# Kernel tuning notes

Hardware: AMD Instinct MI355X
Metric: run time of the kernel (lower is better)

Reference implementation:

```python
import jax, jax.numpy as jnp
import numpy as np

B, N, D = 2, 4096, 2048
H, DH, W = 8, 128, 512          # heads (num_queries), dim_head, window_size
SCALE = 8.0                      # qk_scale (qk_rmsnorm=True)


def setup_inputs() -> dict:
    key = jax.random.key(0)
    ks = jax.random.split(key, 5)
    return {
        "x": jax.random.normal(ks[0], (B, N, D), jnp.float32),
        "Wq": jax.random.normal(ks[1], (H * DH, D), jnp.float32) * 0.02,
        "Wkv": jax.random.normal(ks[2], (2 * H * DH, D), jnp.float32) * 0.02,
        "q_scale": jnp.ones((DH,), jnp.float32),
        "k_scale": jnp.ones((DH,), jnp.float32),
        "Wg": jax.random.normal(ks[3], (H, D), jnp.float32) * 0.02,
        "bg": jnp.zeros((H,), jnp.float32),
        "Wo": jax.random.normal(ks[4], (D, H * DH), jnp.float32) * 0.02,
    }


def _l2norm(t):
    # F.normalize: x / max(||x||, eps)
    return t / jnp.maximum(jnp.linalg.norm(t, axis=-1, keepdims=True), 1e-12)


def reference(x, Wq, Wkv, q_scale, k_scale, Wg, bg, Wo):
    b, n, _ = x.shape
    inner = H * DH
    q = (x @ Wq.T).reshape(b, n, H, DH).transpose(0, 2, 1, 3)      # b h n d
    kv = x @ Wkv.T
    k = kv[..., :inner].reshape(b, n, H, DH).transpose(0, 2, 1, 3)
    v = kv[..., inner:].reshape(b, n, H, DH).transpose(0, 2, 1, 3)
    # qk rmsnorm
    q = _l2norm(q) * q_scale
    k = _l2norm(k) * k_scale

    nb = n // W
    qb = q.reshape(b, H, nb, W, DH)
    kb = k.reshape(b, H, nb, W, DH)
    vb = v.reshape(b, H, nb, W, DH)

    def look_around(t):  # prepend previous bucket (look_backward=1)
        prev = jnp.concatenate([jnp.zeros_like(t[:, :, :1]), t[:, :, :-1]], axis=2)
        return jnp.concatenate([prev, t], axis=3)  # b h nb 2W d

    kw, vw = look_around(kb), look_around(vb)

    pos = jnp.arange(n).reshape(nb, W)
    pos_prev = jnp.concatenate([jnp.full((1, W), -1), pos[:-1]], axis=0)
    posk = jnp.concatenate([pos_prev, pos], axis=1)                 # nb 2W
    dist = pos[:, :, None] - posk[:, None, :]                       # nb W 2W
    # causal + exact window: attend j with 0 <= i - j <= W, valid (non-pad) key
    mask = (posk[:, None, :] >= 0) & (dist >= 0) & (dist <= W)

    sim = jnp.einsum('bhnid,bhnjd->bhnij', qb * SCALE, kw)
    sim = jnp.where(mask, sim, jnp.finfo(sim.dtype).min)
    attn = jax.nn.softmax(sim, axis=-1)
    o = jnp.einsum('bhnij,bhnjd->bhnid', attn, vw).reshape(b, H, n, DH)

    # per-head sigmoid value gating
    gates = jax.nn.sigmoid(jnp.einsum('bnd,hd->bhn', x, Wg) + bg[None, :, None])
    o = o * gates[..., None]

    o = o.transpose(0, 2, 1, 3).reshape(b, n, inner)                # b n (h d)
    return o @ Wo.T
```

## Files before the change

### kernel.cpp

```cpp
#include <hip/hip_runtime.h>
#include <hip/hip_bf16.h>
#include <cstdint>

typedef short short8 __attribute__((ext_vector_type(8)));
typedef __bf16 bf16x8 __attribute__((ext_vector_type(8)));
typedef float f32x4 __attribute__((ext_vector_type(4)));
typedef unsigned short u16;
typedef unsigned int u32;

#define B_  2
#define N_  4096
#define D_  2048
#define H_  8
#define DH_ 128
#define W_  512
#define M_  (B_*N_)
#define INNER_ (H_*DH_)

static __device__ __forceinline__ u16 f2bf(float f) {
  u32 u = __float_as_uint(f);
  u32 r = (u + 0x7fffu + ((u >> 16) & 1u)) >> 16;
  return (u16)r;
}
static __device__ __forceinline__ float bf2f(u16 u) {
  return __uint_as_float(((u32)u) << 16);
}
static __device__ __forceinline__ f32x4 mfma16(short8 a, short8 b, f32x4 c) {
  return __builtin_amdgcn_mfma_f32_16x16x32_bf16(
      __builtin_bit_cast(bf16x8, a), __builtin_bit_cast(bf16x8, b), c, 0, 0, 0);
}

#define GLOAD_LDS16(g, s) \
  __builtin_amdgcn_global_load_lds((const __attribute__((address_space(1))) void*)(g), \
                                   (__attribute__((address_space(3))) void*)(s), 16, 0, 0)

__global__ __launch_bounds__(256) void cvt_kernel(
    const float* __restrict__ x, const float* __restrict__ Wq,
    const float* __restrict__ Wkv, const float* __restrict__ Wo,
    u16* __restrict__ xb, u16* __restrict__ Wcat, u16* __restrict__ Wob) {
  size_t i = ((size_t)blockIdx.x * 256 + threadIdx.x) * 8;
  const float* src; u16* dst; size_t off;
  const size_t SX = 16777216ul, SQ = 2097152ul, SKV = 4194304ul;
  if (i < SX)                { src = x;   dst = xb;             off = i; }
  else if (i < SX+SQ)        { src = Wq;  dst = Wcat;           off = i - SX; }
  else if (i < SX+SQ+SKV)    { src = Wkv; dst = Wcat + 2097152; off = i - SX - SQ; }
  else                       { src = Wo;  dst = Wob;            off = i - SX - SQ - SKV; }
  float4 a = *(const float4*)(src + off);
  float4 b = *(const float4*)(src + off + 4);
  short8 o;
  o[0]=(short)f2bf(a.x); o[1]=(short)f2bf(a.y); o[2]=(short)f2bf(a.z); o[3]=(short)f2bf(a.w);
  o[4]=(short)f2bf(b.x); o[5]=(short)f2bf(b.y); o[6]=(short)f2bf(b.z); o[7]=(short)f2bf(b.w);
  *(short8*)(dst + off) = o;
}

template<int EPI>
__global__ __launch_bounds__(256) void gemm_bt(
    const u16* __restrict__ A, const u16* __restrict__ Bw,
    u16* __restrict__ Dq, u16* __restrict__ Dk, u16* __restrict__ Dv,
    float* __restrict__ Cf, int N, int K) {
  __shared__ u16 sA[128*64];
  __shared__ u16 sB[128*64];
  const int tid = threadIdx.x;
  const int lane = tid & 63, wv = tid >> 6;
  const int wm = wv >> 1, wn = wv & 1;
  const int m0 = blockIdx.y * 128, n0 = blockIdx.x * 128;
  const int l15 = lane & 15, l4 = lane >> 4;
  f32x4 acc[4][4] = {};

  #pragma unroll 1
  for (int kt = 0; kt < K; kt += 64) {
    __syncthreads();
    #pragma unroll
    for (int r = 0; r < 4; ++r) {
      int cf = r*256 + tid;
      int row = cf >> 3, cph = cf & 7;
      int clg = cph ^ (row & 7);
      GLOAD_LDS16(A + (size_t)(m0 + row)*K + kt + clg*8, sA + (size_t)(r*256 + wv*64)*8);
    }
    #pragma unroll
    for (int r = 0; r < 4; ++r) {
      int cf = r*256 + tid;
      int row = cf >> 3, cph = cf & 7;
      int clg = cph ^ (row & 7);
      GLOAD_LDS16(Bw + (size_t)(n0 + row)*K + kt + clg*8, sB + (size_t)(r*256 + wv*64)*8);
    }
    __syncthreads();
    #pragma unroll
    for (int ks = 0; ks < 2; ++ks) {
      short8 af[4], bfr[4];
      #pragma unroll
      for (int mf = 0; mf < 4; ++mf) {
        int row = wm*64 + mf*16 + l15;
        int ch = (ks*4 + l4) ^ (row & 7);
        af[mf] = *(const short8*)(sA + row*64 + ch*8);
      }
      #pragma unroll
      for (int nf = 0; nf < 4; ++nf) {
        int row = wn*64 + nf*16 + l15;
        int ch = (ks*4 + l4) ^ (row & 7);
        bfr[nf] = *(const short8*)(sB + row*64 + ch*8);
      }
      #pragma unroll
      for (int mf = 0; mf < 4; ++mf)
        #pragma unroll
        for (int nf = 0; nf < 4; ++nf)
          acc[mf][nf] = mfma16(af[mf], bfr[nf], acc[mf][nf]);
    }
  }

  if (EPI == 0) {
    const int bufsel = blockIdx.x >> 3;
    const int h = blockIdx.x & 7;
    u16* dst = bufsel == 0 ? Dq : (bufsel == 1 ? Dk : Dv);
    #pragma unroll
    for (int mf = 0; mf < 4; ++mf)
      #pragma unroll
      for (int nf = 0; nf < 4; ++nf)
        #pragma unroll
        for (int j = 0; j < 4; ++j) {
          int m = m0 + wm*64 + mf*16 + l4*4 + j;
          int d = wn*64 + nf*16 + l15;
          int b = m >> 12, n = m & (N_ - 1);
          dst[(((size_t)(b*H_ + h)*N_ + n) << 7) + d] = f2bf(acc[mf][nf][j]);
        }
  } else {
    #pragma unroll
    for (int mf = 0; mf < 4; ++mf)
      #pragma unroll
      for (int nf = 0; nf < 4; ++nf)
        #pragma unroll
        for (int j = 0; j < 4; ++j) {
          int m = m0 + wm*64 + mf*16 + l4*4 + j;
          int nn = n0 + wn*64 + nf*16 + l15;
          Cf[(size_t)m*N + nn] = acc[mf][nf][j];
        }
  }
}

__global__ __launch_bounds__(256) void normqk_kernel(
    u16* __restrict__ qb, u16* __restrict__ kb,
    const float* __restrict__ qs, const float* __restrict__ ks) {
  int lane = threadIdx.x & 63, wv = threadIdx.x >> 6;
  size_t vec = (size_t)blockIdx.x * 4 + wv;
  bool isq = vec < 65536;
  u16* p = isq ? qb + vec*128 : kb + (vec - 65536)*128;
  const float* sc = isq ? qs : ks;
  u32 u = *(const u32*)(p + lane*2);
  float a = bf2f((u16)(u & 0xffffu));
  float b = bf2f((u16)(u >> 16));
  float ss = a*a + b*b;
  #pragma unroll
  for (int off = 32; off >= 1; off >>= 1) ss += __shfl_xor(ss, off);
  float inv = 1.0f / fmaxf(sqrtf(ss), 1e-12f);
  if (isq) inv *= 8.0f;
  float r0 = a * inv * sc[lane*2];
  float r1 = b * inv * sc[lane*2 + 1];
  *(u32*)(p + lane*2) = (u32)f2bf(r0) | ((u32)f2bf(r1) << 16);
}

__global__ __launch_bounds__(256) void transpose_v_kernel(
    const u16* __restrict__ v, u16* __restrict__ vT) {
  int bh = blockIdx.x >> 6;
  int n0 = (blockIdx.x & 63) << 6;
  __shared__ u16 tl[64][136];
  int tid = threadIdx.x;
  #pragma unroll
  for (int r = 0; r < 4; ++r) {
    int cf = r*256 + tid;
    int row = cf >> 4, ch = cf & 15;
    *(short8*)&tl[row][ch*8] = *(const short8*)(v + ((size_t)bh*N_ + n0 + row)*128 + ch*8);
  }
  __syncthreads();
  #pragma unroll
  for (int r = 0; r < 4; ++r) {
    int cf = r*256 + tid;
    int d = cf >> 3, nch = cf & 7;
    short8 o;
    #pragma unroll
    for (int i = 0; i < 8; ++i) o[i] = (short)tl[nch*8 + i][d];
    *(short8*)(vT + ((size_t)bh*128 + d)*N_ + n0 + nch*8) = o;
  }
}

__global__ __launch_bounds__(256) void gates_kernel(
    const float* __restrict__ x, const float* __restrict__ Wg,
    const float* __restrict__ bg, float* __restrict__ gates) {
  int m = blockIdx.x;
  int tid = threadIdx.x;
  const float* xr = x + (size_t)m * D_;
  float acc[8] = {};
  for (int d = tid; d < D_; d += 256) {
    float xv = xr[d];
    #pragma unroll
    for (int h = 0; h < 8; ++h) acc[h] = fmaf(xv, Wg[h*D_ + d], acc[h]);
  }
  #pragma unroll
  for (int h = 0; h < 8; ++h)
    #pragma unroll
    for (int off = 32; off >= 1; off >>= 1) acc[h] += __shfl_xor(acc[h], off);
  __shared__ float red[4][8];
  int lane = tid & 63, wv = tid >> 6;
  if (lane == 0) {
    #pragma unroll
    for (int h = 0; h < 8; ++h) red[wv][h] = acc[h];
  }
  __syncthreads();
  if (tid < 8) {
    float vsum = red[0][tid] + red[1][tid] + red[2][tid] + red[3][tid] + bg[tid];
    gates[(size_t)m*8 + tid] = 1.0f / (1.0f + __expf(-vsum));
  }
}

__global__ __launch_bounds__(256) void attn_kernel(
    const u16* __restrict__ q, const u16* __restrict__ k,
    const u16* __restrict__ vT, const float* __restrict__ gates,
    u16* __restrict__ o) {
  const int bid = blockIdx.x;
  const int t = bid & 3;
  const int c = (bid >> 2) & 7;
  const int bh = bid >> 5;
  const int b = bh >> 3, h = bh & 7;
  const int i0 = c*W_ + t*128;
  const int tid = threadIdx.x;
  const int lane = tid & 63, wv = tid >> 6;
  const int l15 = lane & 15, l4 = lane >> 4;

  __shared__ u16 sK[64*128];
  __shared__ u16 sV[128*64];
  __shared__ u16 sP[4][32*64];

  short8 qf[2][4];
  const u16* qbase = q + (((size_t)bh*N_ + i0 + wv*32) << 7);
  #pragma unroll
  for (int mf = 0; mf < 2; ++mf)
    #pragma unroll
    for (int ks = 0; ks < 4; ++ks)
      qf[mf][ks] = *(const short8*)(qbase + (mf*16 + l15)*128 + ks*32 + l4*8);

  float mrow[2][4], lrow[2][4];
  f32x4 oacc[2][8];
  #pragma unroll
  for (int mf = 0; mf < 2; ++mf) {
    #pragma unroll
    for (int j = 0; j < 4; ++j) { mrow[mf][j] = -1e30f; lrow[mf][j] = 0.f; }
    #pragma unroll
    for (int df = 0; df < 8; ++df) oacc[mf][df] = (f32x4){0.f,0.f,0.f,0.f};
  }
  u16* sPw = &sP[wv][0];

  #pragma unroll 1
  for (int kt = 0; kt < 10; ++kt) {
    const int j0 = i0 - 512 + kt*64;
    if (j0 < 0) continue;
    __syncthreads();
    #pragma unroll
    for (int r = 0; r < 4; ++r) {
      int cf = r*256 + tid;
      int row = cf >> 4, cph = cf & 15;
      int clg = cph ^ (row & 15);
      GLOAD_LDS16(k + (((size_t)bh*N_ + j0 + row) << 7) + clg*8, sK + (size_t)(r*256 + wv*64)*8);
    }
    #pragma unroll
    for (int r = 0; r < 4; ++r) {
      int cf = r*256 + tid;
      int row = cf >> 3, cph = cf & 7;
      int clg = cph ^ (row & 7);
      GLOAD_LDS16(vT + ((size_t)bh*128 + row)*N_ + j0 + clg*8, sV + (size_t)(r*256 + wv*64)*8);
    }
    __syncthreads();

    f32x4 s[2][4];
    #pragma unroll
    for (int mf = 0; mf < 2; ++mf)
      #pragma unroll
      for (int nf = 0; nf < 4; ++nf) s[mf][nf] = (f32x4){0.f,0.f,0.f,0.f};
    #pragma unroll
    for (int ks = 0; ks < 4; ++ks) {
      short8 kb[4];
      #pragma unroll
      for (int nf = 0; nf < 4; ++nf) {
        int row = nf*16 + l15;
        int ch = (ks*4 + l4) ^ (row & 15);
        kb[nf] = *(const short8*)(sK + row*128 + ch*8);
      }
      #pragma unroll
      for (int mf = 0; mf < 2; ++mf)
        #pragma unroll
        for (int nf = 0; nf < 4; ++nf)
          s[mf][nf] = mfma16(qf[mf][ks], kb[nf], s[mf][nf]);
    }

    if (kt < 2 || kt > 7) {
      #pragma unroll
      for (int mf = 0; mf < 2; ++mf)
        #pragma unroll
        for (int nf = 0; nf < 4; ++nf)
          #pragma unroll
          for (int j = 0; j < 4; ++j) {
            int r = wv*32 + mf*16 + l4*4 + j;
            int sidx = nf*16 + l15;
            int dist = (i0 + r) - (j0 + sidx);
            if (dist < 0 || dist > 512) s[mf][nf][j] = -1e30f;
          }
    }

    #pragma unroll
    for (int mf = 0; mf < 2; ++mf) {
      #pragma unroll
      for (int j = 0; j < 4; ++j) {
        float mx = fmaxf(fmaxf(s[mf][0][j], s[mf][1][j]), fmaxf(s[mf][2][j], s[mf][3][j]));
        #pragma unroll
        for (int off = 1; off <= 8; off <<= 1) mx = fmaxf(mx, __shfl_xor(mx, off));
        float mnew = fmaxf(mrow[mf][j], mx);
        float scal = __expf(mrow[mf][j] - mnew);
        mrow[mf][j] = mnew;
        float ls = 0.f;
        #pragma unroll
        for (int nf = 0; nf < 4; ++nf) {
          float p = __expf(s[mf][nf][j] - mnew);
          s[mf][nf][j] = p;
          ls += p;
        }
        #pragma unroll
        for (int off = 1; off <= 8; off <<= 1) ls += __shfl_xor(ls, off);
        lrow[mf][j] = lrow[mf][j]*scal + ls;
        #pragma unroll
        for (int df = 0; df < 8; ++df) oacc[mf][df][j] *= scal;
        int prow = mf*16 + l4*4 + j;
        #pragma unroll
        for (int nf = 0; nf < 4; ++nf) {
          int pcol = nf*16 + l15;
          int ch = (pcol >> 3) ^ (prow & 7);
          sPw[prow*64 + ch*8 + (pcol & 7)] = f2bf(s[mf][nf][j]);
        }
      }
    }

    #pragma unroll
    for (int ks2 = 0; ks2 < 2; ++ks2) {
      short8 pa[2];
      #pragma unroll
      for (int mf = 0; mf < 2; ++mf) {
        int prow = mf*16 + l15;
        int ch = (ks2*4 + l4) ^ (prow & 7);
        pa[mf] = *(const short8*)(sPw + prow*64 + ch*8);
      }
      #pragma unroll
      for (int df = 0; df < 8; ++df) {
        int vd = df*16 + l15;
        int ch2 = (ks2*4 + l4) ^ (vd & 7);
        short8 vb = *(const short8*)(sV + vd*64 + ch2*8);
        #pragma unroll
        for (int mf = 0; mf < 2; ++mf)
          oacc[mf][df] = mfma16(pa[mf], vb, oacc[mf][df]);
      }
    }
  }

  #pragma unroll
  for (int mf = 0; mf < 2; ++mf)
    #pragma unroll
    for (int j = 0; j < 4; ++j) {
      int r = wv*32 + mf*16 + l4*4 + j;
      int i = i0 + r;
      float f = (1.0f / lrow[mf][j]) * gates[((size_t)b*N_ + i)*8 + h];
      #pragma unroll
      for (int df = 0; df < 8; ++df)
        o[((size_t)b*N_ + i)*INNER_ + h*128 + df*16 + l15] = f2bf(oacc[mf][df][j] * f);
    }
}

extern "C" void kernel_launch(void* const* d_in, const int* in_sizes, int n_in,
                              void* d_out, int out_size, void* d_ws, size_t ws_size,
                              hipStream_t stream) {
  const float* x       = (const float*)d_in[0];
  const float* Wq      = (const float*)d_in[1];
  const float* Wkv     = (const float*)d_in[2];
  const float* q_scale = (const float*)d_in[3];
  const float* k_scale = (const float*)d_in[4];
  const float* Wg      = (const float*)d_in[5];
  const float* bg      = (const float*)d_in[6];
  const float* Wo      = (const float*)d_in[7];
  float* out = (float*)d_out;

  u16* qb  = (u16*)d_out;
  u16* kb  = qb + 8388608;
  u16* vb  = kb + 8388608;
  u16* vTb = vb + 8388608;

  char* w = (char*)d_ws;
  u16* xb   = (u16*)w;
  u16* ob   = (u16*)w;
  u16* Wcat = (u16*)(w + 33554432);
  u16* Wob  = (u16*)(w + 46137344);
  float* gb = (float*)(w + 50331648);
  (void)in_sizes; (void)n_in; (void)out_size; (void)ws_size;

  cvt_kernel<<<12288, 256, 0, stream>>>(x, Wq, Wkv, Wo, xb, Wcat, Wob);
  gemm_bt<0><<<dim3(24, 64), 256, 0, stream>>>(xb, Wcat, qb, kb, vb, nullptr, 3072, 2048);
  normqk_kernel<<<32768, 256, 0, stream>>>(qb, kb, q_scale, k_scale);
  transpose_v_kernel<<<1024, 256, 0, stream>>>(vb, vTb);
  gates_kernel<<<8192, 256, 0, stream>>>(x, Wg, bg, gb);
  attn_kernel<<<512, 256, 0, stream>>>(qb, kb, vTb, gb, ob);
  gemm_bt<1><<<dim3(16, 64), 256, 0, stream>>>(ob, Wob, nullptr, nullptr, nullptr, out, 2048, 1024);
}
```

Measured before the change: 314.7 us.

## Replace GEMM with 256x256-tile, 8-wave, multi-stage pipelined LDS kernel

Replaces the 128x128 single-buffered GEMM with a 256x256 tile, 512-thread kernel. It uses 128 KB of dynamic LDS split into three stages of 32-wide K half-tiles, issues global-to-LDS prefetches interleaved with the MFMA phases, and raises MFMA priority with s_setprio. Blocks are remapped with an XCD-aware swizzle for L2 locality, and the QKV epilogue now derives head and buffer per column. The goal is to hide load latency and raise arithmetic intensity in both projection GEMMs. In exchange the kernel has heavier register and LDS pressure and relies on hand-placed waitcnt and barrier choreography with hardcoded grid assumptions (by = swz & 31).

Result: faster. 308.3 us (-2.1%).

```diff
diff --git a/kernel.cpp b/kernel.cpp
--- a/kernel.cpp
+++ b/kernel.cpp
@@ -53,86 +53,121 @@
   *(short8*)(dst + off) = o;
 }
 
+#define BARRIER() __builtin_amdgcn_s_barrier()
+#define WAIT_LGKM0() do { asm volatile("s_waitcnt lgkmcnt(0)" ::: "memory"); \
+                          __builtin_amdgcn_sched_barrier(0); } while(0)
+#define WAIT_VM4() asm volatile("s_waitcnt vmcnt(4)" ::: "memory")
+#define WAIT_VM0() asm volatile("s_waitcnt vmcnt(0)" ::: "memory")
+
+#define STAGE_HALF(gbase, sreg) do { \
+    const u16* _g = (gbase) + _cs; \
+    GLOAD_LDS16(_g + (size_t)(wv*32 + (lane>>2))*K,      (sreg) + wv*1024); \
+    GLOAD_LDS16(_g + (size_t)(wv*32 + 16 + (lane>>2))*K, (sreg) + wv*1024 + 512); \
+  } while(0)
+
+#define LOAD_AF(sreg, mfb) do { \
+    _Pragma("unroll") for (int q = 0; q < 4; ++q) \
+      af[q] = *(const short8*)((sreg) + (wm*128 + ((mfb)+q)*16 + l15)*32 + fch); \
+  } while(0)
+#define LOAD_BF(sreg) do { \
+    _Pragma("unroll") for (int q = 0; q < 4; ++q) \
+      bf[q] = *(const short8*)((sreg) + (wn*64 + q*16 + l15)*32 + fch); \
+  } while(0)
+
+#define PH_MFMA(mfb) do { \
+    __builtin_amdgcn_s_setprio(1); \
+    _Pragma("unroll") for (int q = 0; q < 4; ++q) \
+      _Pragma("unroll") for (int nf = 0; nf < 4; ++nf) \
+        acc[(mfb)+q][nf] = mfma16(af[q], bf[nf], acc[(mfb)+q][nf]); \
+    __builtin_amdgcn_s_setprio(0); \
+  } while(0)
+
+#define TILE4(T, SA_C, SB_C, SA_N, SB_N, C1, C2) do { \
+    const u16* gAt = gA + (size_t)(T)*64; \
+    const u16* gBt = gB + (size_t)(T)*64; \
+    short8 af[4], bf[4]; \
+    LOAD_AF(SA_C, 0); LOAD_BF(SB_C); \
+    if (C1) STAGE_HALF(gAt + 96, (SA_N) + 8192); \
+    BARRIER(); WAIT_LGKM0(); PH_MFMA(0); BARRIER(); \
+    LOAD_AF(SA_C, 4); \
+    if (C1) STAGE_HALF(gBt + 96, (SB_N) + 8192); \
+    BARRIER(); WAIT_LGKM0(); PH_MFMA(4); BARRIER(); \
+    LOAD_AF((SA_C) + 8192, 0); LOAD_BF((SB_C) + 8192); \
+    if (C2) STAGE_HALF(gAt + 128, SA_C); \
+    BARRIER(); WAIT_LGKM0(); PH_MFMA(0); BARRIER(); \
+    LOAD_AF((SA_C) + 8192, 4); \
+    if (C2) { STAGE_HALF(gBt + 128, SB_C); WAIT_VM4(); } else { WAIT_VM0(); } \
+    BARRIER(); WAIT_LGKM0(); PH_MFMA(4); BARRIER(); \
+  } while(0)
+
 template<int EPI>
-__global__ __launch_bounds__(256) void gemm_bt(
+__global__ __launch_bounds__(512, 2) void gemm256(
     const u16* __restrict__ A, const u16* __restrict__ Bw,
     u16* __restrict__ Dq, u16* __restrict__ Dk, u16* __restrict__ Dv,
-    float* __restrict__ Cf, int N, int K) {
-  __shared__ u16 sA[128*64];
-  __shared__ u16 sB[128*64];
+    float* __restrict__ Cf, int Ncols, int K) {
+  extern __shared__ u16 lds[];
   const int tid = threadIdx.x;
   const int lane = tid & 63, wv = tid >> 6;
-  const int wm = wv >> 1, wn = wv & 1;
-  const int m0 = blockIdx.y * 128, n0 = blockIdx.x * 128;
+  const int wm = wv >> 2, wn = wv & 3;
   const int l15 = lane & 15, l4 = lane >> 4;
-  f32x4 acc[4][4] = {};
-
+
+  const int nwg = gridDim.x;
+  const int swz = (blockIdx.x & 7) * (nwg >> 3) + (blockIdx.x >> 3);
+  const int by = swz & 31;
+  const int bx = swz >> 5;
+  const int m0 = by << 8, n0 = bx << 8;
+
+  const u16* gA = A + (size_t)m0 * K;
+  const u16* gB = Bw + (size_t)n0 * K;
+  u16* sA0 = lds;
+  u16* sB0 = lds + 32768;
+
+  const int _cs = ((lane & 3) ^ ((lane >> 3) & 3)) * 8;
+  const int fch = (l4 ^ ((l15 >> 1) & 3)) * 8;
+
+  f32x4 acc[8][4] = {};
+
+  STAGE_HALF(gA,      sA0);
+  STAGE_HALF(gB,      sB0);
+  STAGE_HALF(gA + 32, sA0 + 8192);
+  STAGE_HALF(gB + 32, sB0 + 8192);
+  STAGE_HALF(gA + 64, sA0 + 16384);
+  STAGE_HALF(gB + 64, sB0 + 16384);
+  WAIT_VM4();
+  BARRIER();
+
+  const int nt = K >> 6;
   #pragma unroll 1
-  for (int kt = 0; kt < K; kt += 64) {
-    __syncthreads();
-    #pragma unroll
-    for (int r = 0; r < 4; ++r) {
-      int cf = r*256 + tid;
-      int row = cf >> 3, cph = cf & 7;
-      int clg = cph ^ (row & 7);
-      GLOAD_LDS16(A + (size_t)(m0 + row)*K + kt + clg*8, sA + (size_t)(r*256 + wv*64)*8);
-    }
-    #pragma unroll
-    for (int r = 0; r < 4; ++r) {
-      int cf = r*256 + tid;
-      int row = cf >> 3, cph = cf & 7;
-      int clg = cph ^ (row & 7);
-      GLOAD_LDS16(Bw + (size_t)(n0 + row)*K + kt + clg*8, sB + (size_t)(r*256 + wv*64)*8);
-    }
-    __syncthreads();
-    #pragma unroll
-    for (int ks = 0; ks < 2; ++ks) {
-      short8 af[4], bfr[4];
-      #pragma unroll
-      for (int mf = 0; mf < 4; ++mf) {
-        int row = wm*64 + mf*16 + l15;
-        int ch = (ks*4 + l4) ^ (row & 7);
-        af[mf] = *(const short8*)(sA + row*64 + ch*8);
-      }
-      #pragma unroll
-      for (int nf = 0; nf < 4; ++nf) {
-        int row = wn*64 + nf*16 + l15;
-        int ch = (ks*4 + l4) ^ (row & 7);
-        bfr[nf] = *(const short8*)(sB + row*64 + ch*8);
-      }
-      #pragma unroll
-      for (int mf = 0; mf < 4; ++mf)
-        #pragma unroll
-        for (int nf = 0; nf < 4; ++nf)
-          acc[mf][nf] = mfma16(af[mf], bfr[nf], acc[mf][nf]);
-    }
+  for (int t = 0; t < nt; t += 2) {
+    const bool c2 = t + 2 < nt, c3 = t + 3 < nt;
+    TILE4(t,     sA0,         sB0,         sA0 + 16384, sB0 + 16384, true, c2);
+    TILE4(t + 1, sA0 + 16384, sB0 + 16384, sA0,         sB0,         c2,   c3);
   }
 
   if (EPI == 0) {
-    const int bufsel = blockIdx.x >> 3;
-    const int h = blockIdx.x & 7;
-    u16* dst = bufsel == 0 ? Dq : (bufsel == 1 ? Dk : Dv);
-    #pragma unroll
-    for (int mf = 0; mf < 4; ++mf)
+    #pragma unroll
+    for (int mf = 0; mf < 8; ++mf)
       #pragma unroll
       for (int nf = 0; nf < 4; ++nf)
         #pragma unroll
         for (int j = 0; j < 4; ++j) {
-          int m = m0 + wm*64 + mf*16 + l4*4 + j;
-          int d = wn*64 + nf*16 + l15;
+          int m = m0 + wm*128 + mf*16 + l4*4 + j;
+          int gc = n0 + wn*64 + nf*16 + l15;
+          int bufsel = gc >> 10, inner = gc & 1023, h = inner >> 7, d = inner & 127;
+          u16* dst = bufsel == 0 ? Dq : (bufsel == 1 ? Dk : Dv);
           int b = m >> 12, n = m & (N_ - 1);
           dst[(((size_t)(b*H_ + h)*N_ + n) << 7) + d] = f2bf(acc[mf][nf][j]);
         }
   } else {
     #pragma unroll
-    for (int mf = 0; mf < 4; ++mf)
+    for (int mf = 0; mf < 8; ++mf)
       #pragma unroll
       for (int nf = 0; nf < 4; ++nf)
         #pragma unroll
         for (int j = 0; j < 4; ++j) {
-          int m = m0 + wm*64 + mf*16 + l4*4 + j;
-          int nn = n0 + wn*64 + nf*16 + l15;
-          Cf[(size_t)m*N + nn] = acc[mf][nf][j];
+          int m = m0 + wm*128 + mf*16 + l4*4 + j;
+          int gc = n0 + wn*64 + nf*16 + l15;
+          Cf[(size_t)m*Ncols + gc] = acc[mf][nf][j];
         }
   }
 }
@@ -396,11 +431,16 @@
   float* gb = (float*)(w + 50331648);
   (void)in_sizes; (void)n_in; (void)out_size; (void)ws_size;
 
+  hipFuncSetAttribute((const void*)gemm256<0>,
+                      hipFuncAttributeMaxDynamicSharedMemorySize, 131072);
+  hipFuncSetAttribute((const void*)gemm256<1>,
+                      hipFuncAttributeMaxDynamicSharedMemorySize, 131072);
+
   cvt_kernel<<<12288, 256, 0, stream>>>(x, Wq, Wkv, Wo, xb, Wcat, Wob);
-  gemm_bt<0><<<dim3(24, 64), 256, 0, stream>>>(xb, Wcat, qb, kb, vb, nullptr, 3072, 2048);
+  gemm256<0><<<384, 512, 131072, stream>>>(xb, Wcat, qb, kb, vb, nullptr, 3072, 2048);
   normqk_kernel<<<32768, 256, 0, stream>>>(qb, kb, q_scale, k_scale);
   transpose_v_kernel<<<1024, 256, 0, stream>>>(vb, vTb);
   gates_kernel<<<8192, 256, 0, stream>>>(x, Wg, bg, gb);
   attn_kernel<<<512, 256, 0, stream>>>(qb, kb, vTb, gb, ob);
-  gemm_bt<1><<<dim3(16, 64), 256, 0, stream>>>(ob, Wob, nullptr, nullptr, nullptr, out, 2048, 1024);
-}
+  gemm256<1><<<256, 512, 131072, stream>>>(ob, Wob, nullptr, nullptr, nullptr, out, 2048, 1024);
+}
```

## Double-buffer K/V tiles in attention, skip masked tiles, read bf16 x in gates

Applied to the files above, without the earlier changes.

Attention now prefetches the next K/V tile into a second LDS buffer while computing on the current one, using dynamic shared memory, with one barrier per iteration. Each wave skips compute for key tiles that are fully outside its causal window. The gates kernel reads the already-converted bf16 copy of x instead of fp32, halving its memory traffic at a small precision cost. The larger LDS footprint may limit occupancy.

New measurement: 314.4 us. No clear change (-0.1%).

```diff
diff --git a/kernel.cpp b/kernel.cpp
--- a/kernel.cpp
+++ b/kernel.cpp
@@ -183,16 +183,20 @@
 }
 
 __global__ __launch_bounds__(256) void gates_kernel(
-    const float* __restrict__ x, const float* __restrict__ Wg,
+    const u16* __restrict__ xb, const float* __restrict__ Wg,
     const float* __restrict__ bg, float* __restrict__ gates) {
   int m = blockIdx.x;
   int tid = threadIdx.x;
-  const float* xr = x + (size_t)m * D_;
+  const u16* xr = xb + (size_t)m * D_;
   float acc[8] = {};
-  for (int d = tid; d < D_; d += 256) {
-    float xv = xr[d];
-    #pragma unroll
-    for (int h = 0; h < 8; ++h) acc[h] = fmaf(xv, Wg[h*D_ + d], acc[h]);
+  for (int d0 = tid*8; d0 < D_; d0 += 256*8) {
+    short8 xv8 = *(const short8*)(xr + d0);
+    #pragma unroll
+    for (int e = 0; e < 8; ++e) {
+      float xv = bf2f((u16)xv8[e]);
+      #pragma unroll
+      for (int h = 0; h < 8; ++h) acc[h] = fmaf(xv, Wg[h*D_ + d0 + e], acc[h]);
+    }
   }
   #pragma unroll
   for (int h = 0; h < 8; ++h)
@@ -215,6 +219,9 @@
     const u16* __restrict__ q, const u16* __restrict__ k,
     const u16* __restrict__ vT, const float* __restrict__ gates,
     u16* __restrict__ o) {
+  extern __shared__ u16 alds[];
+  u16* sK = alds;
+  u16* sV = alds + 16384;
   const int bid = blockIdx.x;
   const int t = bid & 3;
   const int c = (bid >> 2) & 7;
@@ -224,10 +231,23 @@
   const int tid = threadIdx.x;
   const int lane = tid & 63, wv = tid >> 6;
   const int l15 = lane & 15, l4 = lane >> 4;
-
-  __shared__ u16 sK[64*128];
-  __shared__ u16 sV[128*64];
-  __shared__ u16 sP[4][32*64];
+  u16* sPw = alds + 32768 + wv*2048;
+
+#define STAGE_KV(KT, PB) do { \
+    const int _j0 = i0 - 512 + (KT)*64; \
+    u16* _dK = sK + (PB)*8192; \
+    u16* _dV = sV + (PB)*8192; \
+    _Pragma("unroll") for (int r = 0; r < 4; ++r) { \
+      int cf = r*256 + tid; int row = cf >> 4, cph = cf & 15; \
+      int clg = cph ^ (row & 15); \
+      GLOAD_LDS16(k + (((size_t)bh*N_ + _j0 + row) << 7) + clg*8, _dK + (size_t)(r*256 + wv*64)*8); \
+    } \
+    _Pragma("unroll") for (int r = 0; r < 4; ++r) { \
+      int cf = r*256 + tid; int row = cf >> 3, cph = cf & 7; \
+      int clg = cph ^ (row & 7); \
+      GLOAD_LDS16(vT + ((size_t)bh*128 + row)*N_ + _j0 + clg*8, _dV + (size_t)(r*256 + wv*64)*8); \
+    } \
+  } while(0)
 
   short8 qf[2][4];
   const u16* qbase = q + (((size_t)bh*N_ + i0 + wv*32) << 7);
@@ -246,115 +266,110 @@
     #pragma unroll
     for (int df = 0; df < 8; ++df) oacc[mf][df] = (f32x4){0.f,0.f,0.f,0.f};
   }
-  u16* sPw = &sP[wv][0];
+
+  const int kt0 = (i0 >= 512) ? 0 : ((512 - i0) >> 6);
+  STAGE_KV(kt0, 0);
+  __syncthreads();
 
   #pragma unroll 1
-  for (int kt = 0; kt < 10; ++kt) {
+  for (int kt = kt0; kt < 10; ++kt) {
+    const int pb = (kt - kt0) & 1;
+    if (kt < 9) STAGE_KV(kt + 1, pb ^ 1);
     const int j0 = i0 - 512 + kt*64;
-    if (j0 < 0) continue;
-    __syncthreads();
-    #pragma unroll
-    for (int r = 0; r < 4; ++r) {
-      int cf = r*256 + tid;
-      int row = cf >> 4, cph = cf & 15;
-      int clg = cph ^ (row & 15);
-      GLOAD_LDS16(k + (((size_t)bh*N_ + j0 + row) << 7) + clg*8, sK + (size_t)(r*256 + wv*64)*8);
-    }
-    #pragma unroll
-    for (int r = 0; r < 4; ++r) {
-      int cf = r*256 + tid;
-      int row = cf >> 3, cph = cf & 7;
-      int clg = cph ^ (row & 7);
-      GLOAD_LDS16(vT + ((size_t)bh*128 + row)*N_ + j0 + clg*8, sV + (size_t)(r*256 + wv*64)*8);
-    }
-    __syncthreads();
-
-    f32x4 s[2][4];
-    #pragma unroll
-    for (int mf = 0; mf < 2; ++mf)
-      #pragma unroll
-      for (int nf = 0; nf < 4; ++nf) s[mf][nf] = (f32x4){0.f,0.f,0.f,0.f};
-    #pragma unroll
-    for (int ks = 0; ks < 4; ++ks) {
-      short8 kb[4];
-      #pragma unroll
-      for (int nf = 0; nf < 4; ++nf) {
-        int row = nf*16 + l15;
-        int ch = (ks*4 + l4) ^ (row & 15);
-        kb[nf] = *(const short8*)(sK + row*128 + ch*8);
-      }
+    const int base = 512 - kt*64;
+    const int rmin = wv*32;
+    if (base + rmin + 31 >= 0 && base + rmin - 63 <= 512) {
+      const u16* cK = sK + pb*8192;
+      const u16* cV = sV + pb*8192;
+
+      f32x4 s[2][4];
       #pragma unroll
       for (int mf = 0; mf < 2; ++mf)
         #pragma unroll
-        for (int nf = 0; nf < 4; ++nf)
-          s[mf][nf] = mfma16(qf[mf][ks], kb[nf], s[mf][nf]);
-    }
-
-    if (kt < 2 || kt > 7) {
-      #pragma unroll
-      for (int mf = 0; mf < 2; ++mf)
-        #pragma unroll
-        for (int nf = 0; nf < 4; ++nf)
-          #pragma unroll
-          for (int j = 0; j < 4; ++j) {
-            int r = wv*32 + mf*16 + l4*4 + j;
-            int sidx = nf*16 + l15;
-            int dist = (i0 + r) - (j0 + sidx);
-            if (dist < 0 || dist > 512) s[mf][nf][j] = -1e30f;
+        for (int nf = 0; nf < 4; ++nf) s[mf][nf] = (f32x4){0.f,0.f,0.f,0.f};
+      #pragma unroll
+      for (int ks = 0; ks < 4; ++ks) {
+        short8 kb[4];
+        #pragma unroll
+        for (int nf = 0; nf < 4; ++nf) {
+          int row = nf*16 + l15;
+          int ch = (ks*4 + l4) ^ (row & 15);
+          kb[nf] = *(const short8*)(cK + row*128 + ch*8);
+        }
+        #pragma unroll
+        for (int mf = 0; mf < 2; ++mf)
+          #pragma unroll
+          for (int nf = 0; nf < 4; ++nf)
+            s[mf][nf] = mfma16(qf[mf][ks], kb[nf], s[mf][nf]);
+      }
+
+      if (kt < 2 || kt > 7) {
+        #pragma unroll
+        for (int mf = 0; mf < 2; ++mf)
+          #pragma unroll
+          for (int nf = 0; nf < 4; ++nf)
+            #pragma unroll
+            for (int j = 0; j < 4; ++j) {
+              int r = wv*32 + mf*16 + l4*4 + j;
+              int sidx = nf*16 + l15;
+              int dist = (i0 + r) - (j0 + sidx);
+              if (dist < 0 || dist > 512) s[mf][nf][j] = -1e30f;
+            }
+      }
+
+      #pragma unroll
+      for (int mf = 0; mf < 2; ++mf) {
+        #pragma unroll
+        for (int j = 0; j < 4; ++j) {
+          float mx = fmaxf(fmaxf(s[mf][0][j], s[mf][1][j]), fmaxf(s[mf][2][j], s[mf][3][j]));
+          #pragma unroll
+          for (int off = 1; off <= 8; off <<= 1) mx = fmaxf(mx, __shfl_xor(mx, off));
+          float mnew = fmaxf(mrow[mf][j], mx);
+          float scal = __expf(mrow[mf][j] - mnew);
+          mrow[mf][j] = mnew;
+          float ls = 0.f;
+          #pragma unroll
+          for (int nf = 0; nf < 4; ++nf) {
+            float p = __expf(s[mf][nf][j] - mnew);
+            s[mf][nf][j] = p;
+            ls += p;
           }
-    }
-
-    #pragma unroll
-    for (int mf = 0; mf < 2; ++mf) {
-      #pragma unroll
-      for (int j = 0; j < 4; ++j) {
-        float mx = fmaxf(fmaxf(s[mf][0][j], s[mf][1][j]), fmaxf(s[mf][2][j], s[mf][3][j]));
-        #pragma unroll
-        for (int off = 1; off <= 8; off <<= 1) mx = fmaxf(mx, __shfl_xor(mx, off));
-        float mnew = fmaxf(mrow[mf][j], mx);
-        float scal = __expf(mrow[mf][j] - mnew);
-        mrow[mf][j] = mnew;
-        float ls = 0.f;
-        #pragma unroll
-        for (int nf = 0; nf < 4; ++nf) {
-          float p = __expf(s[mf][nf][j] - mnew);
-          s[mf][nf][j] = p;
-          ls += p;
-        }
-        #pragma unroll
-        for (int off = 1; off <= 8; off <<= 1) ls += __shfl_xor(ls, off);
-        lrow[mf][j] = lrow[mf][j]*scal + ls;
-        #pragma unroll
-        for (int df = 0; df < 8; ++df) oacc[mf][df][j] *= scal;
-        int prow = mf*16 + l4*4 + j;
-        #pragma unroll
-        for (int nf = 0; nf < 4; ++nf) {
-          int pcol = nf*16 + l15;
-          int ch = (pcol >> 3) ^ (prow & 7);
-          sPw[prow*64 + ch*8 + (pcol & 7)] = f2bf(s[mf][nf][j]);
-        }
-      }
-    }
-
-    #pragma unroll
-    for (int ks2 = 0; ks2 < 2; ++ks2) {
-      short8 pa[2];
-      #pragma unroll
-      for (int mf = 0; mf < 2; ++mf) {
-        int prow = mf*16 + l15;
-        int ch = (ks2*4 + l4) ^ (prow & 7);
-        pa[mf] = *(const short8*)(sPw + prow*64 + ch*8);
-      }
-      #pragma unroll
-      for (int df = 0; df < 8; ++df) {
-        int vd = df*16 + l15;
-        int ch2 = (ks2*4 + l4) ^ (vd & 7);
-        short8 vb = *(const short8*)(sV + vd*64 + ch2*8);
-        #pragma unroll
-        for (int mf = 0; mf < 2; ++mf)
-          oacc[mf][df] = mfma16(pa[mf], vb, oacc[mf][df]);
-      }
-    }
+          #pragma unroll
+          for (int off = 1; off <= 8; off <<= 1) ls += __shfl_xor(ls, off);
+          lrow[mf][j] = lrow[mf][j]*scal + ls;
+          #pragma unroll
+          for (int df = 0; df < 8; ++df) oacc[mf][df][j] *= scal;
+          int prow = mf*16 + l4*4 + j;
+          #pragma unroll
+          for (int nf = 0; nf < 4; ++nf) {
+            int pcol = nf*16 + l15;
+            int ch = (pcol >> 3) ^ (prow & 7);
+            sPw[prow*64 + ch*8 + (pcol & 7)] = f2bf(s[mf][nf][j]);
+          }
+        }
+      }
+
+      #pragma unroll
+      for (int ks2 = 0; ks2 < 2; ++ks2) {
+        short8 pa[2];
+        #pragma unroll
+        for (int mf = 0; mf < 2; ++mf) {
+          int prow = mf*16 + l15;
+          int ch = (ks2*4 + l4) ^ (prow & 7);
+          pa[mf] = *(const short8*)(sPw + prow*64 + ch*8);
+        }
+        #pragma unroll
+        for (int df = 0; df < 8; ++df) {
+          int vd = df*16 + l15;
+          int ch2 = (ks2*4 + l4) ^ (vd & 7);
+          short8 vb = *(const short8*)(cV + vd*64 + ch2*8);
+          #pragma unroll
+          for (int mf = 0; mf < 2; ++mf)
+            oacc[mf][df] = mfma16(pa[mf], vb, oacc[mf][df]);
+        }
+      }
+    }
+    if (kt < 9) __syncthreads();
   }
 
   #pragma unroll
@@ -368,6 +383,7 @@
       for (int df = 0; df < 8; ++df)
         o[((size_t)b*N_ + i)*INNER_ + h*128 + df*16 + l15] = f2bf(oacc[mf][df][j] * f);
     }
+#undef STAGE_KV
 }
 
 extern "C" void kernel_launch(void* const* d_in, const int* in_sizes, int n_in,
@@ -396,11 +412,14 @@
   float* gb = (float*)(w + 50331648);
   (void)in_sizes; (void)n_in; (void)out_size; (void)ws_size;
 
+  hipFuncSetAttribute((const void*)attn_kernel,
+                      hipFuncAttributeMaxDynamicSharedMemorySize, 81920);
+
   cvt_kernel<<<12288, 256, 0, stream>>>(x, Wq, Wkv, Wo, xb, Wcat, Wob);
   gemm_bt<0><<<dim3(24, 64), 256, 0, stream>>>(xb, Wcat, qb, kb, vb, nullptr, 3072, 2048);
   normqk_kernel<<<32768, 256, 0, stream>>>(qb, kb, q_scale, k_scale);
   transpose_v_kernel<<<1024, 256, 0, stream>>>(vb, vTb);
-  gates_kernel<<<8192, 256, 0, stream>>>(x, Wg, bg, gb);
-  attn_kernel<<<512, 256, 0, stream>>>(qb, kb, vTb, gb, ob);
+  gates_kernel<<<8192, 256, 0, stream>>>(xb, Wg, bg, gb);
+  attn_kernel<<<512, 256, 81920, stream>>>(qb, kb, vTb, gb, ob);
   gemm_bt<1><<<dim3(16, 64), 256, 0, stream>>>(ob, Wob, nullptr, nullptr, nullptr, out, 2048, 1024);
 }
```

## Fuse QK l2-norm and V transpose into projection GEMM epilogues

Applied to the files above, without the earlier changes.

Splits the QKV projection GEMM into three launches whose epilogues apply the per-row l2 normalization and scale (Q, K) or write V directly transposed, removing the separate normqk and transpose_v kernels and their extra memory round-trips. The gates kernel now reads bf16 x instead of fp32, halving its input traffic at a small precision cost. The attention loop also skips score computation for wave sub-tiles that fall entirely outside the causal window. The trade-off is three smaller GEMM grids instead of one, plus a shared-memory reduction and barrier in the epilogue.

New measurement: 323.5 us. +2.8%, slower.

```diff
diff --git a/kernel.cpp b/kernel.cpp
--- a/kernel.cpp
+++ b/kernel.cpp
@@ -3,6 +3,7 @@
 #include <cstdint>
 
 typedef short short8 __attribute__((ext_vector_type(8)));
+typedef short short4v __attribute__((ext_vector_type(4)));
 typedef __bf16 bf16x8 __attribute__((ext_vector_type(8)));
 typedef float f32x4 __attribute__((ext_vector_type(4)));
 typedef unsigned short u16;
@@ -56,10 +57,11 @@
 template<int EPI>
 __global__ __launch_bounds__(256) void gemm_bt(
     const u16* __restrict__ A, const u16* __restrict__ Bw,
-    u16* __restrict__ Dq, u16* __restrict__ Dk, u16* __restrict__ Dv,
-    float* __restrict__ Cf, int N, int K) {
+    u16* __restrict__ Dst, float* __restrict__ Cf,
+    const float* __restrict__ sc, int K) {
   __shared__ u16 sA[128*64];
   __shared__ u16 sB[128*64];
+  __shared__ float pbuf[2][128];
   const int tid = threadIdx.x;
   const int lane = tid & 63, wv = tid >> 6;
   const int wm = wv >> 1, wn = wv & 1;
@@ -108,21 +110,53 @@
     }
   }
 
-  if (EPI == 0) {
-    const int bufsel = blockIdx.x >> 3;
-    const int h = blockIdx.x & 7;
-    u16* dst = bufsel == 0 ? Dq : (bufsel == 1 ? Dk : Dv);
+  if (EPI <= 1) {
     #pragma unroll
     for (int mf = 0; mf < 4; ++mf)
       #pragma unroll
-      for (int nf = 0; nf < 4; ++nf)
-        #pragma unroll
-        for (int j = 0; j < 4; ++j) {
-          int m = m0 + wm*64 + mf*16 + l4*4 + j;
+      for (int j = 0; j < 4; ++j) {
+        float ss = acc[mf][0][j]*acc[mf][0][j] + acc[mf][1][j]*acc[mf][1][j]
+                 + acc[mf][2][j]*acc[mf][2][j] + acc[mf][3][j]*acc[mf][3][j];
+        #pragma unroll
+        for (int off = 1; off <= 8; off <<= 1) ss += __shfl_xor(ss, off);
+        if (l15 == 0) pbuf[wn][wm*64 + mf*16 + l4*4 + j] = ss;
+      }
+    __syncthreads();
+    const int h = blockIdx.x;
+    const int b = m0 >> 12;
+    #pragma unroll
+    for (int mf = 0; mf < 4; ++mf)
+      #pragma unroll
+      for (int j = 0; j < 4; ++j) {
+        int rloc = wm*64 + mf*16 + l4*4 + j;
+        float ss = pbuf[0][rloc] + pbuf[1][rloc];
+        float inv = 1.0f / fmaxf(sqrtf(ss), 1e-12f);
+        if (EPI == 0) inv *= 8.0f;
+        int n = (m0 + rloc) & (N_ - 1);
+        size_t base = ((size_t)(b*H_ + h)*N_ + n) << 7;
+        #pragma unroll
+        for (int nf = 0; nf < 4; ++nf) {
           int d = wn*64 + nf*16 + l15;
-          int b = m >> 12, n = m & (N_ - 1);
-          dst[(((size_t)(b*H_ + h)*N_ + n) << 7) + d] = f2bf(acc[mf][nf][j]);
+          Dst[base + d] = f2bf(acc[mf][nf][j] * inv * sc[d]);
         }
+      }
+  } else if (EPI == 2) {
+    const int h = blockIdx.x;
+    const int b = m0 >> 12;
+    const int bh = b*H_ + h;
+    #pragma unroll
+    for (int mf = 0; mf < 4; ++mf)
+      #pragma unroll
+      for (int nf = 0; nf < 4; ++nf) {
+        int d = wn*64 + nf*16 + l15;
+        int n = ((m0 & (N_ - 1)) + wm*64 + mf*16 + l4*4);
+        short4v pk;
+        pk[0] = (short)f2bf(acc[mf][nf][0]);
+        pk[1] = (short)f2bf(acc[mf][nf][1]);
+        pk[2] = (short)f2bf(acc[mf][nf][2]);
+        pk[3] = (short)f2bf(acc[mf][nf][3]);
+        *(short4v*)(Dst + ((size_t)bh*128 + d)*N_ + n) = pk;
+      }
   } else {
     #pragma unroll
     for (int mf = 0; mf < 4; ++mf)
@@ -132,67 +166,26 @@
         for (int j = 0; j < 4; ++j) {
           int m = m0 + wm*64 + mf*16 + l4*4 + j;
           int nn = n0 + wn*64 + nf*16 + l15;
-          Cf[(size_t)m*N + nn] = acc[mf][nf][j];
+          Cf[(size_t)m*D_ + nn] = acc[mf][nf][j];
         }
   }
 }
 
-__global__ __launch_bounds__(256) void normqk_kernel(
-    u16* __restrict__ qb, u16* __restrict__ kb,
-    const float* __restrict__ qs, const float* __restrict__ ks) {
-  int lane = threadIdx.x & 63, wv = threadIdx.x >> 6;
-  size_t vec = (size_t)blockIdx.x * 4 + wv;
-  bool isq = vec < 65536;
-  u16* p = isq ? qb + vec*128 : kb + (vec - 65536)*128;
-  const float* sc = isq ? qs : ks;
-  u32 u = *(const u32*)(p + lane*2);
-  float a = bf2f((u16)(u & 0xffffu));
-  float b = bf2f((u16)(u >> 16));
-  float ss = a*a + b*b;
-  #pragma unroll
-  for (int off = 32; off >= 1; off >>= 1) ss += __shfl_xor(ss, off);
-  float inv = 1.0f / fmaxf(sqrtf(ss), 1e-12f);
-  if (isq) inv *= 8.0f;
-  float r0 = a * inv * sc[lane*2];
-  float r1 = b * inv * sc[lane*2 + 1];
-  *(u32*)(p + lane*2) = (u32)f2bf(r0) | ((u32)f2bf(r1) << 16);
-}
-
-__global__ __launch_bounds__(256) void transpose_v_kernel(
-    const u16* __restrict__ v, u16* __restrict__ vT) {
-  int bh = blockIdx.x >> 6;
-  int n0 = (blockIdx.x & 63) << 6;
-  __shared__ u16 tl[64][136];
-  int tid = threadIdx.x;
-  #pragma unroll
-  for (int r = 0; r < 4; ++r) {
-    int cf = r*256 + tid;
-    int row = cf >> 4, ch = cf & 15;
-    *(short8*)&tl[row][ch*8] = *(const short8*)(v + ((size_t)bh*N_ + n0 + row)*128 + ch*8);
-  }
-  __syncthreads();
-  #pragma unroll
-  for (int r = 0; r < 4; ++r) {
-    int cf = r*256 + tid;
-    int d = cf >> 3, nch = cf & 7;
-    short8 o;
-    #pragma unroll
-    for (int i = 0; i < 8; ++i) o[i] = (short)tl[nch*8 + i][d];
-    *(short8*)(vT + ((size_t)bh*128 + d)*N_ + n0 + nch*8) = o;
-  }
-}
-
 __global__ __launch_bounds__(256) void gates_kernel(
-    const float* __restrict__ x, const float* __restrict__ Wg,
+    const u16* __restrict__ xb, const float* __restrict__ Wg,
     const float* __restrict__ bg, float* __restrict__ gates) {
   int m = blockIdx.x;
   int tid = threadIdx.x;
-  const float* xr = x + (size_t)m * D_;
+  const u16* xr = xb + (size_t)m * D_;
   float acc[8] = {};
-  for (int d = tid; d < D_; d += 256) {
-    float xv = xr[d];
-    #pragma unroll
-    for (int h = 0; h < 8; ++h) acc[h] = fmaf(xv, Wg[h*D_ + d], acc[h]);
+  for (int d0 = tid*8; d0 < D_; d0 += 256*8) {
+    short8 xv8 = *(const short8*)(xr + d0);
+    #pragma unroll
+    for (int e = 0; e < 8; ++e) {
+      float xv = bf2f((u16)xv8[e]);
+      #pragma unroll
+      for (int h = 0; h < 8; ++h) acc[h] = fmaf(xv, Wg[h*D_ + d0 + e], acc[h]);
+    }
   }
   #pragma unroll
   for (int h = 0; h < 8; ++h)
@@ -269,6 +262,10 @@
     }
     __syncthreads();
 
+    const int base = 512 - kt*64;
+    const int rmin = wv*32;
+    if (base + rmin + 31 < 0 || base + rmin - 63 > 512) continue;
+
     f32x4 s[2][4];
     #pragma unroll
     for (int mf = 0; mf < 2; ++mf)
@@ -385,8 +382,7 @@
 
   u16* qb  = (u16*)d_out;
   u16* kb  = qb + 8388608;
-  u16* vb  = kb + 8388608;
-  u16* vTb = vb + 8388608;
+  u16* vTb = kb + 8388608;
 
   char* w = (char*)d_ws;
   u16* xb   = (u16*)w;
@@ -397,10 +393,10 @@
   (void)in_sizes; (void)n_in; (void)out_size; (void)ws_size;
 
   cvt_kernel<<<12288, 256, 0, stream>>>(x, Wq, Wkv, Wo, xb, Wcat, Wob);
-  gemm_bt<0><<<dim3(24, 64), 256, 0, stream>>>(xb, Wcat, qb, kb, vb, nullptr, 3072, 2048);
-  normqk_kernel<<<32768, 256, 0, stream>>>(qb, kb, q_scale, k_scale);
-  transpose_v_kernel<<<1024, 256, 0, stream>>>(vb, vTb);
-  gates_kernel<<<8192, 256, 0, stream>>>(x, Wg, bg, gb);
+  gemm_bt<0><<<dim3(8, 64), 256, 0, stream>>>(xb, Wcat,                       qb,  nullptr, q_scale, 2048);
+  gemm_bt<1><<<dim3(8, 64), 256, 0, stream>>>(xb, Wcat + (size_t)1024*2048,   kb,  nullptr, k_scale, 2048);
+  gemm_bt<2><<<dim3(8, 64), 256, 0, stream>>>(xb, Wcat + (size_t)2048*2048,   vTb, nullptr, nullptr, 2048);
+  gates_kernel<<<8192, 256, 0, stream>>>(xb, Wg, bg, gb);
   attn_kernel<<<512, 256, 0, stream>>>(qb, kb, vTb, gb, ob);
-  gemm_bt<1><<<dim3(16, 64), 256, 0, stream>>>(ob, Wob, nullptr, nullptr, nullptr, out, 2048, 1024);
-}
+  gemm_bt<3><<<dim3(16, 64), 256, 0, stream>>>(ob, Wob, nullptr, out, nullptr, 1024);
+}
```
